# Optimization experiments

Hardware: AMD Instinct MI355X
Metric: run time of the kernel (lower is better)

Reference implementation:

```python
import jax, jax.numpy as jnp
import numpy as np

N_NODES = 10000
N_EDGES = 320000


def gcn_conv(x, edge_index, edge_weight, W, b):
    """PyG GCNConv (add_self_loops=True, normalize=True) with edge weights.
    x: [N, Fin], edge_index: [2, E] (row=source, col=target), W: [Fin, Fout].
    """
    n = x.shape[0]
    row, col = edge_index[0], edge_index[1]
    # add self-loops with weight 1
    loop = jnp.arange(n, dtype=edge_index.dtype)
    row = jnp.concatenate([row, loop])
    col = jnp.concatenate([col, loop])
    ew = jnp.concatenate([edge_weight, jnp.ones((n,), dtype=edge_weight.dtype)])
    # symmetric normalization: D^-1/2 A D^-1/2
    deg = jax.ops.segment_sum(ew, col, num_segments=n)
    dinv = jnp.where(deg > 0, jax.lax.rsqrt(deg), 0.0)
    norm = dinv[row] * ew * dinv[col]  # [E+N]
    # linear transform first (smaller of the two widths often), then aggregate
    xw = x @ W  # [N, Fout]
    msg = norm[:, None] * xw[row]  # [E+N, Fout] gather
    out = jax.ops.segment_sum(msg, col, num_segments=n)  # scatter-add
    return out + b


def setup_inputs() -> dict:
    key = jax.random.key(0)
    ks = jax.random.split(key, 8)
    F = 256
    x = jax.random.normal(ks[0], (N_NODES, F), dtype=jnp.float32)
    edge_index = jax.random.randint(ks[1], (2, N_EDGES), 0, N_NODES, dtype=jnp.int64)
    edge_weights = jax.random.uniform(ks[2], (N_EDGES,), dtype=jnp.float32)
    s1 = 1.0 / np.sqrt(F)
    s2 = 1.0 / np.sqrt(2 * F)
    s3 = 1.0 / np.sqrt(3 * F)
    W1 = jax.random.normal(ks[3], (F, 2 * F), dtype=jnp.float32) * s1
    b1 = jnp.zeros((2 * F,), dtype=jnp.float32)
    W2 = jax.random.normal(ks[4], (2 * F, 3 * F), dtype=jnp.float32) * s2
    b2 = jnp.zeros((3 * F,), dtype=jnp.float32)
    W3 = jax.random.normal(ks[5], (3 * F, 8), dtype=jnp.float32) * s3
    b3 = jnp.zeros((8,), dtype=jnp.float32)
    return {"x": x, "edge_index": edge_index, "edge_weights": edge_weights,
            "W1": W1, "b1": b1, "W2": W2, "b2": b2, "W3": W3, "b3": b3}


def reference(x, edge_index, edge_weights, W1, b1, W2, b2, W3, b3):
    h = jax.nn.relu(gcn_conv(x, edge_index, edge_weights, W1, b1))
    h = jax.nn.relu(gcn_conv(h, edge_index, edge_weights, W2, b2))
    return gcn_conv(h, edge_index, edge_weights, W3, b3)
```

## Files before the change

### kernel.cpp

```cpp
#include <hip/hip_runtime.h>

#define N_NODES 10000
#define N_EDGES 320000
#define ELL_CAP 88
#define ELL_TOT (N_NODES * ELL_CAP)
#define CDL 8

__device__ __forceinline__ unsigned short f2h_bits(float v) {
    _Float16 h = (_Float16)v;
    unsigned short u;
    __builtin_memcpy(&u, &h, 2);
    return u;
}
__device__ __forceinline__ float h2f_lo(unsigned int g) {
    unsigned short u = (unsigned short)(g & 0xFFFFu);
    _Float16 h; __builtin_memcpy(&h, &u, 2);
    return (float)h;
}
__device__ __forceinline__ float h2f_hi(unsigned int g) {
    unsigned short u = (unsigned short)(g >> 16);
    _Float16 h; __builtin_memcpy(&h, &u, 2);
    return (float)h;
}

__device__ __forceinline__ int cd_cnt(unsigned long long v) { return (int)(v >> 32); }
__device__ __forceinline__ float cd_deg(unsigned long long v) {
    return 1.0f + (float)(unsigned int)(v & 0xFFFFFFFFull) * 5.9604645e-8f;
}

__global__ __launch_bounds__(256) void setup_kernel(
        unsigned long long* __restrict__ cda,
        uint2* __restrict__ ell_e,
        const float* __restrict__ x, unsigned short* __restrict__ xh,
        const float* __restrict__ W1, unsigned short* __restrict__ w1t,
        const float* __restrict__ W2, unsigned short* __restrict__ w2t) {
    int i = blockIdx.x * 256 + threadIdx.x;
    const int S0 = N_NODES;
    const int S1 = S0 + ELL_TOT;
    const int S2 = S1 + N_NODES * 256;
    const int S3 = S2 + 256 * 512;
    const int S4 = S3 + 512 * 768;
    if (i < S0) {
        cda[i * CDL] = 0ULL;
    } else if (i < S1) {
        int j = i - S0;
        uint2 z; z.x = 0u; z.y = 0u;
        ell_e[j] = z;
    } else if (i < S2) {
        int j = i - S1;
        xh[j] = f2h_bits(x[j]);
    } else if (i < S3) {
        int j = i - S2;
        int k = j >> 9, n = j & 511;
        w1t[n * 256 + k] = f2h_bits(W1[j]);
    } else if (i < S4) {
        int j = i - S3;
        int k = j / 768, n = j - k * 768;
        w2t[n * 512 + k] = f2h_bits(W2[j]);
    }
}

__global__ __launch_bounds__(256) void ell_fill_kernel(const int* __restrict__ row,
                                                       const int* __restrict__ col,
                                                       const float* __restrict__ ew,
                                                       unsigned long long* __restrict__ cda,
                                                       uint2* __restrict__ ell_e, int e) {
    int i = blockIdx.x * 256 + threadIdx.x;
    if (i < e) {
        int c = col[i];
        float w = ew[i];
        unsigned long long inc =
            (1ULL << 32) | (unsigned long long)__float2uint_rn(w * 16777216.0f);
        unsigned long long old = atomicAdd(cda + c * CDL, inc);
        int slot = (int)(old >> 32);
        if (slot < ELL_CAP) {
            uint2 p;
            p.x = (unsigned int)row[i];
            p.y = __float_as_uint(w);
            ell_e[c * ELL_CAP + slot] = p;
        }
    }
}

template <int F, int SSHIFT, bool RAW>
__global__ __launch_bounds__(256) void agg_ell_kernel(const unsigned int* __restrict__ xpk,
                                                      const unsigned long long* __restrict__ cda,
                                                      const uint2* __restrict__ ell_e,
                                                      uint2* __restrict__ ell_n,
                                                      unsigned int* __restrict__ o) {
    constexpr int F2 = F / 2;
    const int b = (int)blockIdx.x;
    const int slice = b & ((1 << SSHIFT) - 1);
    const int node = __builtin_amdgcn_readfirstlane(
        (b >> SSHIFT) * 4 + ((int)threadIdx.x >> 6));
    const int lane = (int)threadIdx.x & 63;
    const int f2 = slice * 64 + lane;
    const unsigned long long cv = cda[node * CDL];
    const float srn = rsqrtf(cd_deg(cv));
    const float si = srn * srn;
    unsigned int gs = xpk[node * F2 + f2];
    float acc0 = si * h2f_lo(gs);
    float acc1 = si * h2f_hi(gs);
    const int base = node * ELL_CAP;
    int cnt8 = (cd_cnt(cv) + 7) & ~7;
    if (cnt8 > ELL_CAP) cnt8 = ELL_CAP;

    const int* meta = (const int*)(RAW ? ell_e : (const uint2*)ell_n);

    for (int j = 0; j < cnt8; j += 8) {
        const int* ep = meta + (size_t)(base + j) * 2;
        int4 a0 = *(const int4*)(ep + 0);
        int4 a1 = *(const int4*)(ep + 4);
        int4 a2 = *(const int4*)(ep + 8);
        int4 a3 = *(const int4*)(ep + 12);
        unsigned int g0 = xpk[a0.x * F2 + f2];
        unsigned int g1 = xpk[a0.z * F2 + f2];
        unsigned int g2 = xpk[a1.x * F2 + f2];
        unsigned int g3 = xpk[a1.z * F2 + f2];
        unsigned int g4 = xpk[a2.x * F2 + f2];
        unsigned int g5 = xpk[a2.z * F2 + f2];
        unsigned int g6 = xpk[a3.x * F2 + f2];
        unsigned int g7 = xpk[a3.z * F2 + f2];

        float w0, w1, w2, w3, w4, w5, w6, w7;
        if constexpr (RAW) {
            w0 = rsqrtf(cd_deg(cda[a0.x * CDL])) * __int_as_float(a0.y) * srn;
            w1 = rsqrtf(cd_deg(cda[a0.z * CDL])) * __int_as_float(a0.w) * srn;
            w2 = rsqrtf(cd_deg(cda[a1.x * CDL])) * __int_as_float(a1.y) * srn;
            w3 = rsqrtf(cd_deg(cda[a1.z * CDL])) * __int_as_float(a1.w) * srn;
            w4 = rsqrtf(cd_deg(cda[a2.x * CDL])) * __int_as_float(a2.y) * srn;
            w5 = rsqrtf(cd_deg(cda[a2.z * CDL])) * __int_as_float(a2.w) * srn;
            w6 = rsqrtf(cd_deg(cda[a3.x * CDL])) * __int_as_float(a3.y) * srn;
            w7 = rsqrtf(cd_deg(cda[a3.z * CDL])) * __int_as_float(a3.w) * srn;
            if (slice == 0 && lane == 0) {
                uint2* wp = ell_n + base + j;
                uint2 p;
                p.x = (unsigned int)a0.x; p.y = __float_as_uint(w0); wp[0] = p;
                p.x = (unsigned int)a0.z; p.y = __float_as_uint(w1); wp[1] = p;
                p.x = (unsigned int)a1.x; p.y = __float_as_uint(w2); wp[2] = p;
                p.x = (unsigned int)a1.z; p.y = __float_as_uint(w3); wp[3] = p;
                p.x = (unsigned int)a2.x; p.y = __float_as_uint(w4); wp[4] = p;
                p.x = (unsigned int)a2.z; p.y = __float_as_uint(w5); wp[5] = p;
                p.x = (unsigned int)a3.x; p.y = __float_as_uint(w6); wp[6] = p;
                p.x = (unsigned int)a3.z; p.y = __float_as_uint(w7); wp[7] = p;
            }
        } else {
            w0 = __int_as_float(a0.y); w1 = __int_as_float(a0.w);
            w2 = __int_as_float(a1.y); w3 = __int_as_float(a1.w);
            w4 = __int_as_float(a2.y); w5 = __int_as_float(a2.w);
            w6 = __int_as_float(a3.y); w7 = __int_as_float(a3.w);
        }

        acc0 += w0 * h2f_lo(g0) + w1 * h2f_lo(g1) + w2 * h2f_lo(g2) + w3 * h2f_lo(g3);
        acc1 += w0 * h2f_hi(g0) + w1 * h2f_hi(g1) + w2 * h2f_hi(g2) + w3 * h2f_hi(g3);
        acc0 += w4 * h2f_lo(g4) + w5 * h2f_lo(g5) + w6 * h2f_lo(g6) + w7 * h2f_lo(g7);
        acc1 += w4 * h2f_hi(g4) + w5 * h2f_hi(g5) + w6 * h2f_hi(g6) + w7 * h2f_hi(g7);
    }

    unsigned short h0 = f2h_bits(acc0);
    unsigned short h1 = f2h_bits(acc1);
    o[node * F2 + f2] = ((unsigned int)h1 << 16) | h0;
}

typedef _Float16 half8 __attribute__((ext_vector_type(8)));
typedef float f32x4 __attribute__((ext_vector_type(4)));

#define TM 128
#define TN 128
#define BK 32
#define LDS_A 0
#define LDS_B 8192
#define LDS_BUF 16384

__device__ __forceinline__ void async16(const unsigned short* g, unsigned char* l) {
    __builtin_amdgcn_global_load_lds(
        (const __attribute__((address_space(1))) unsigned int*)g,
        (__attribute__((address_space(3))) unsigned int*)l, 16, 0, 0);
}

__global__ __launch_bounds__(256, 3) void gemm_mfma_kernel(
        const unsigned short* __restrict__ A,
        const unsigned short* __restrict__ Bt,
        const float* __restrict__ bias,
        unsigned short* __restrict__ Cb,
        int M, int K, int N) {
    __shared__ unsigned char lds[2 * LDS_BUF];
    const int t = (int)threadIdx.x;

    const int gx = (int)gridDim.x;
    const int nwg = gx * (int)gridDim.y;
    const int lin = (int)blockIdx.y * gx + (int)blockIdx.x;
    const int xcd = lin & 7, idx = lin >> 3;
    const int q = nwg >> 3, r = nwg & 7;
    const int logi = (xcd < r ? xcd * (q + 1) : r * (q + 1) + (xcd - r) * q) + idx;
    const int bm = (logi / gx) * TM;
    const int bn = (logi % gx) * TN;

    const int lane = t & 63;
    const int wave = t >> 6;
    const int wm = (wave & 1) * 64;
    const int wn = (wave >> 1) * 64;

    const int slr = lane >> 2;
    const int scc = (lane & 3) ^ ((slr >> 1) & 3);
    const int bi0 = wave * 2, bi1 = wave * 2 + 1;
    const unsigned short* gA0 = A + (size_t)(bm + bi0 * 16 + slr) * K + scc * 8;
    const unsigned short* gA1 = A + (size_t)(bm + bi1 * 16 + slr) * K + scc * 8;
    const unsigned short* gB0 = Bt + (size_t)(bn + bi0 * 16 + slr) * K + scc * 8;
    const unsigned short* gB1 = Bt + (size_t)(bn + bi1 * 16 + slr) * K + scc * 8;

    const int quad = lane >> 4;
    const int lr16 = lane & 15;
    const int fs = (quad ^ ((lr16 >> 1) & 3)) * 16;

    f32x4 acc[4][4];
    const f32x4 zero4 = {0.f, 0.f, 0.f, 0.f};
#pragma unroll
    for (int i = 0; i < 4; ++i)
#pragma unroll
        for (int j = 0; j < 4; ++j) acc[i][j] = zero4;

    const int KT = K / BK;

    auto stage = [&](int kt, int buf) {
        const int k0 = kt * BK;
        unsigned char* b = &lds[buf * LDS_BUF];
        async16(gA0 + k0, b + LDS_A + bi0 * 1024);
        async16(gA1 + k0, b + LDS_A + bi1 * 1024);
        async16(gB0 + k0, b + LDS_B + bi0 * 1024);
        async16(gB1 + k0, b + LDS_B + bi1 * 1024);
    };

    stage(0, 0);
    __syncthreads();

    for (int kt = 0; kt < KT; ++kt) {
        const int buf = kt & 1;
        if (kt + 1 < KT) stage(kt + 1, buf ^ 1);

        unsigned char* b = &lds[buf * LDS_BUF];
        half8 av[4], bv[4];
#pragma unroll
        for (int i = 0; i < 4; ++i) {
            int ro = (wm + i * 16 + lr16) * 64 + fs;
            av[i] = *(const half8*)(b + LDS_A + ro);
        }
#pragma unroll
        for (int j = 0; j < 4; ++j) {
            int ro = (wn + j * 16 + lr16) * 64 + fs;
            bv[j] = *(const half8*)(b + LDS_B + ro);
        }
#pragma unroll
        for (int i = 0; i < 4; ++i)
#pragma unroll
            for (int j = 0; j < 4; ++j)
                acc[i][j] = __builtin_amdgcn_mfma_f32_16x16x32_f16(av[i], bv[j], acc[i][j], 0, 0, 0);
        __syncthreads();
    }

    float bcol[4];
#pragma unroll
    for (int j = 0; j < 4; ++j) bcol[j] = bias[bn + wn + j * 16 + lr16];
#pragma unroll
    for (int i = 0; i < 4; ++i) {
#pragma unroll
        for (int r2 = 0; r2 < 4; ++r2) {
            int m = bm + wm + i * 16 + quad * 4 + r2;
            if (m < M) {
#pragma unroll
                for (int j = 0; j < 4; ++j) {
                    float vv = fmaxf(acc[i][j][r2] + bcol[j], 0.f);
                    Cb[(size_t)m * N + bn + wn + j * 16 + lr16] = f2h_bits(vv);
                }
            }
        }
    }
}

__global__ __launch_bounds__(64) void gemm_n8_kernel(const unsigned int* __restrict__ Apk,
                                                     const float* __restrict__ B,
                                                     float* __restrict__ C) {
    const int m = blockIdx.x;
    const int lane = (int)threadIdx.x;
    const unsigned int* a = Apk + m * 384;
    float acc[8] = {};
#pragma unroll
    for (int it = 0; it < 6; ++it) {
        int j2 = lane + it * 64;
        unsigned int av = a[j2];
        float a0 = h2f_lo(av), a1 = h2f_hi(av);
        const float* B0 = B + (size_t)(2 * j2) * 8;
        float4 p0 = *(const float4*)(B0);
        float4 p1 = *(const float4*)(B0 + 4);
        float4 q0 = *(const float4*)(B0 + 8);
        float4 q1 = *(const float4*)(B0 + 12);
        acc[0] += a0 * p0.x + a1 * q0.x; acc[1] += a0 * p0.y + a1 * q0.y;
        acc[2] += a0 * p0.z + a1 * q0.z; acc[3] += a0 * p0.w + a1 * q0.w;
        acc[4] += a0 * p1.x + a1 * q1.x; acc[5] += a0 * p1.y + a1 * q1.y;
        acc[6] += a0 * p1.z + a1 * q1.z; acc[7] += a0 * p1.w + a1 * q1.w;
    }
#pragma unroll
    for (int off = 32; off > 0; off >>= 1) {
#pragma unroll
        for (int i = 0; i < 8; ++i) acc[i] += __shfl_down(acc[i], off);
    }
    if (lane == 0) {
#pragma unroll
        for (int i = 0; i < 8; ++i) C[(size_t)m * 8 + i] = acc[i];
    }
}

__global__ __launch_bounds__(64) void agg8_kernel(const float* __restrict__ xw,
                                                  const unsigned long long* __restrict__ cda,
                                                  const uint2* __restrict__ ell_n,
                                                  const float* __restrict__ bias,
                                                  float* __restrict__ out) {
    int node = blockIdx.x;
    int lane = threadIdx.x;
    float acc[8] = {};
    const int base = node * ELL_CAP;
    const unsigned long long cv = cda[node * CDL];
    int cnt = cd_cnt(cv);
    if (cnt > ELL_CAP) cnt = ELL_CAP;
    for (int j = lane; j < cnt; j += 64) {
        uint2 p = ell_n[base + j];
        int src = (int)p.x;
        float w = __uint_as_float(p.y);
        float4 g0 = *(const float4*)(xw + (size_t)src * 8);
        float4 g1 = *(const float4*)(xw + (size_t)src * 8 + 4);
        acc[0] += w * g0.x; acc[1] += w * g0.y; acc[2] += w * g0.z; acc[3] += w * g0.w;
        acc[4] += w * g1.x; acc[5] += w * g1.y; acc[6] += w * g1.z; acc[7] += w * g1.w;
    }
#pragma unroll
    for (int off = 32; off > 0; off >>= 1) {
#pragma unroll
        for (int i = 0; i < 8; ++i) acc[i] += __shfl_down(acc[i], off);
    }
    if (lane == 0) {
        float si = 1.0f / cd_deg(cv);
#pragma unroll
        for (int i = 0; i < 8; ++i)
            out[(size_t)node * 8 + i] = acc[i] + si * xw[(size_t)node * 8 + i] + bias[i];
    }
}


extern "C" void kernel_launch(void* const* d_in, const int* in_sizes, int n_in,
                              void* d_out, int out_size, void* d_ws, size_t ws_size,
                              hipStream_t stream) {
    const int N = N_NODES, E = N_EDGES;
    const int N_PAD = ((N + TM - 1) / TM) * TM;
    const float* x   = (const float*)d_in[0];
    const int*   ei  = (const int*)d_in[1];
    const float* ew  = (const float*)d_in[2];
    const float* W1  = (const float*)d_in[3];
    const float* b1  = (const float*)d_in[4];
    const float* W2  = (const float*)d_in[5];
    const float* b2  = (const float*)d_in[6];
    const float* W3  = (const float*)d_in[7];
    const float* b3  = (const float*)d_in[8];
    float* out = (float*)d_out;

    const int* row = ei;
    const int* col = ei + E;

    char* ws = (char*)d_ws;
    size_t off = 0;
    auto alloc = [&](size_t bytes) {
        void* p = ws + off;
        off += (bytes + 255) & ~(size_t)255;
        return p;
    };
    unsigned long long* cda = (unsigned long long*)alloc((size_t)N * CDL * 8);
    uint2*          ell_e   = (uint2*)alloc((size_t)ELL_TOT * 8);
    uint2*          ell_n   = (uint2*)alloc((size_t)ELL_TOT * 8);
    unsigned short* xh      = (unsigned short*)alloc((size_t)N * 256 * 2);
    unsigned short* h1h     = (unsigned short*)alloc((size_t)N * 512 * 2);
    unsigned short* h2h     = (unsigned short*)alloc((size_t)N * 768 * 2);
    unsigned short* Aagg    = (unsigned short*)alloc((size_t)N_PAD * 512 * 2);
    unsigned short* W1t     = (unsigned short*)alloc((size_t)512 * 256 * 2);
    unsigned short* W2t     = (unsigned short*)alloc((size_t)768 * 512 * 2);
    float*          xw8     = (float*)alloc((size_t)N * 8 * 4);
    (void)ws_size;

    {
        int tot = N + ELL_TOT + N * 256 + 256 * 512 + 512 * 768;
        setup_kernel<<<(tot + 255) / 256, 256, 0, stream>>>(
            cda, ell_e, x, xh, W1, W1t, W2, W2t);
    }
    ell_fill_kernel<<<(E + 255) / 256, 256, 0, stream>>>(row, col, ew, cda, ell_e, E);

    agg_ell_kernel<256, 1, true><<<N * 2 / 4, 256, 0, stream>>>(
        (const unsigned int*)xh, cda, ell_e, ell_n, (unsigned int*)Aagg);
    {
        dim3 grid(512 / TN, N_PAD / TM);
        gemm_mfma_kernel<<<grid, 256, 0, stream>>>(Aagg, W1t, b1, h1h, N, 256, 512);
    }
    agg_ell_kernel<512, 2, false><<<N * 4 / 4, 256, 0, stream>>>(
        (const unsigned int*)h1h, cda, ell_n, ell_n, (unsigned int*)Aagg);
    {
        dim3 grid(768 / TN, N_PAD / TM);
        gemm_mfma_kernel<<<grid, 256, 0, stream>>>(Aagg, W2t, b2, h2h, N, 512, 768);
    }
    gemm_n8_kernel<<<N, 64, 0, stream>>>((const unsigned int*)h2h, W3, xw8);
    agg8_kernel<<<N, 64, 0, stream>>>(xw8, cda, ell_n, b3, out);

    (void)out_size; (void)n_in; (void)in_sizes;
}
```

Before: 202.2 us.

## Fuse layer-3 W3 projection into layer-2 GEMM epilogue with partial sums

The layer-2 MFMA GEMM epilogue now multiplies its ReLU output tile by the matching rows of W3. It reduces across lanes and waves through shuffles and LDS, and writes per-column-tile partial 8-wide projections. This removes the fp16 h2 intermediate write/read and the separate gemm_n8 launch. The final aggregation kernel now sums six partial buffers per gathered source, which multiplies its gather traffic. The epilogue also contains some dead statements.

Measured after the change: 203.1 us. No clear change (+0.4%).

```diff
diff --git a/kernel.cpp b/kernel.cpp
--- a/kernel.cpp
+++ b/kernel.cpp
@@ -171,6 +171,7 @@
 #define LDS_A 0
 #define LDS_B 8192
 #define LDS_BUF 16384
+#define NP 10112
 
 __device__ __forceinline__ void async16(const unsigned short* g, unsigned char* l) {
     __builtin_amdgcn_global_load_lds(
@@ -178,11 +179,14 @@
         (__attribute__((address_space(3))) unsigned int*)l, 16, 0, 0);
 }
 
+template <bool FUSE_W3>
 __global__ __launch_bounds__(256, 3) void gemm_mfma_kernel(
         const unsigned short* __restrict__ A,
         const unsigned short* __restrict__ Bt,
         const float* __restrict__ bias,
         unsigned short* __restrict__ Cb,
+        const float* __restrict__ W3,
+        float* __restrict__ xw8p,
         int M, int K, int N) {
     __shared__ unsigned char lds[2 * LDS_BUF];
     const int t = (int)threadIdx.x;
@@ -261,56 +265,99 @@
     float bcol[4];
 #pragma unroll
     for (int j = 0; j < 4; ++j) bcol[j] = bias[bn + wn + j * 16 + lr16];
-#pragma unroll
-    for (int i = 0; i < 4; ++i) {
-#pragma unroll
-        for (int r2 = 0; r2 < 4; ++r2) {
-            int m = bm + wm + i * 16 + quad * 4 + r2;
-            if (m < M) {
+
+    if constexpr (!FUSE_W3) {
+#pragma unroll
+        for (int i = 0; i < 4; ++i) {
+#pragma unroll
+            for (int r2 = 0; r2 < 4; ++r2) {
+                int m = bm + wm + i * 16 + quad * 4 + r2;
+                if (m < M) {
+#pragma unroll
+                    for (int j = 0; j < 4; ++j) {
+                        float vv = fmaxf(acc[i][j][r2] + bcol[j], 0.f);
+                        Cb[(size_t)m * N + bn + wn + j * 16 + lr16] = f2h_bits(vv);
+                    }
+                }
+            }
+        }
+    } else {
+        const int ct = bn / TN;
+        float* red = (float*)lds;
+        float4 w3a[4], w3b[4];
+#pragma unroll
+        for (int j = 0; j < 4; ++j) {
+            const float* wr = W3 + (size_t)(bn + wn + j * 16 + lr16) * 8;
+            w3a[j] = *(const float4*)wr;
+            w3b[j] = *(const float4*)(wr + 4);
+        }
+#pragma unroll
+        for (int i = 0; i < 4; ++i) {
+#pragma unroll
+            for (int r2 = 0; r2 < 4; ++r2) {
+                float s0 = 0.f, s1 = 0.f, s2 = 0.f, s3 = 0.f;
+                float s4 = 0.f, s5 = 0.f, s6 = 0.f, s7 = 0.f;
 #pragma unroll
                 for (int j = 0; j < 4; ++j) {
                     float vv = fmaxf(acc[i][j][r2] + bcol[j], 0.f);
-                    Cb[(size_t)m * N + bn + wn + j * 16 + lr16] = f2h_bits(vv);
+                    s0 += vv * w3a[j].x; s1 += vv * w3a[j].y;
+                    s2 += vv * w3a[j].z; s3 += vv * w3a[j].w;
+                    s4 += vv * w3b[j].x; s5 += vv * w3b[j].y;
+                    s6 += vv * w3b[j].z; s7 += vv * w3b[j].w;
+                }
+#pragma unroll
+                for (int mk = 1; mk < 16; mk <<= 1) {
+                    s0 += __shfl_xor(s0, mk); s1 += __shfl_xor(s1, mk);
+                    s2 += __shfl_xor(s2, mk); s3 += __shfl_xor(s3, mk);
+                    s4 += __shfl_xor(s4, mk); s5 += __shfl_xor(s5, mk);
+                    s6 += __shfl_xor(s6, mk); s7 += __shfl_xor(s7, mk);
+                }
+                if (wn == 64 && lr16 == 0) {
+                    int rl = wm + i * 16 + quad * 4 + r2;
+                    float* rp = red + rl * 8;
+                    rp[0] = s0; rp[1] = s1; rp[2] = s2; rp[3] = s3;
+                    rp[4] = s4; rp[5] = s5; rp[6] = s6; rp[7] = s7;
+                }
+                acc[i][0][r2] = s0; acc[i][1][r2] = s1;
+                acc[i][2][r2] = s2; acc[i][3][r2] = s3;
+                bcol[0] = bcol[0];
+                if (wn == 0) {
+                }
+                if (wn == 0 && lr16 == 0) {
+                    int rl = wm + i * 16 + quad * 4 + r2;
+                    float* rp = red + 1024 + rl * 8;
+                    rp[0] = s4; rp[1] = s5; rp[2] = s6; rp[3] = s7;
                 }
             }
         }
-    }
-}
-
-__global__ __launch_bounds__(64) void gemm_n8_kernel(const unsigned int* __restrict__ Apk,
-                                                     const float* __restrict__ B,
-                                                     float* __restrict__ C) {
-    const int m = blockIdx.x;
-    const int lane = (int)threadIdx.x;
-    const unsigned int* a = Apk + m * 384;
-    float acc[8] = {};
-#pragma unroll
-    for (int it = 0; it < 6; ++it) {
-        int j2 = lane + it * 64;
-        unsigned int av = a[j2];
-        float a0 = h2f_lo(av), a1 = h2f_hi(av);
-        const float* B0 = B + (size_t)(2 * j2) * 8;
-        float4 p0 = *(const float4*)(B0);
-        float4 p1 = *(const float4*)(B0 + 4);
-        float4 q0 = *(const float4*)(B0 + 8);
-        float4 q1 = *(const float4*)(B0 + 12);
-        acc[0] += a0 * p0.x + a1 * q0.x; acc[1] += a0 * p0.y + a1 * q0.y;
-        acc[2] += a0 * p0.z + a1 * q0.z; acc[3] += a0 * p0.w + a1 * q0.w;
-        acc[4] += a0 * p1.x + a1 * q1.x; acc[5] += a0 * p1.y + a1 * q1.y;
-        acc[6] += a0 * p1.z + a1 * q1.z; acc[7] += a0 * p1.w + a1 * q1.w;
-    }
-#pragma unroll
-    for (int off = 32; off > 0; off >>= 1) {
-#pragma unroll
-        for (int i = 0; i < 8; ++i) acc[i] += __shfl_down(acc[i], off);
-    }
-    if (lane == 0) {
-#pragma unroll
-        for (int i = 0; i < 8; ++i) C[(size_t)m * 8 + i] = acc[i];
-    }
-}
-
-__global__ __launch_bounds__(64) void agg8_kernel(const float* __restrict__ xw,
+        __syncthreads();
+        if (wn == 0 && lr16 == 0) {
+#pragma unroll
+            for (int i = 0; i < 4; ++i) {
+#pragma unroll
+                for (int r2 = 0; r2 < 4; ++r2) {
+                    int rl = wm + i * 16 + quad * 4 + r2;
+                    int m = bm + rl;
+                    if (m < M) {
+                        const float* pp = red + rl * 8;
+                        const float* sp = red + 1024 + rl * 8;
+                        float* xp = xw8p + ((size_t)ct * NP + m) * 8;
+                        xp[0] = acc[i][0][r2] + pp[0];
+                        xp[1] = acc[i][1][r2] + pp[1];
+                        xp[2] = acc[i][2][r2] + pp[2];
+                        xp[3] = acc[i][3][r2] + pp[3];
+                        xp[4] = sp[0] + pp[4];
+                        xp[5] = sp[1] + pp[5];
+                        xp[6] = sp[2] + pp[6];
+                        xp[7] = sp[3] + pp[7];
+                    }
+                }
+            }
+        }
+    }
+}
+
+__global__ __launch_bounds__(64) void agg8_kernel(const float* __restrict__ xw8p,
                                                   const unsigned long long* __restrict__ cda,
                                                   const uint2* __restrict__ ell_n,
                                                   const float* __restrict__ bias,
@@ -326,10 +373,18 @@
         uint2 p = ell_n[base + j];
         int src = (int)p.x;
         float w = __uint_as_float(p.y);
-        float4 g0 = *(const float4*)(xw + (size_t)src * 8);
-        float4 g1 = *(const float4*)(xw + (size_t)src * 8 + 4);
-        acc[0] += w * g0.x; acc[1] += w * g0.y; acc[2] += w * g0.z; acc[3] += w * g0.w;
-        acc[4] += w * g1.x; acc[5] += w * g1.y; acc[6] += w * g1.z; acc[7] += w * g1.w;
+        float s0 = 0.f, s1 = 0.f, s2 = 0.f, s3 = 0.f;
+        float s4 = 0.f, s5 = 0.f, s6 = 0.f, s7 = 0.f;
+#pragma unroll
+        for (int ct = 0; ct < 6; ++ct) {
+            const float* xp = xw8p + ((size_t)ct * NP + src) * 8;
+            float4 g0 = *(const float4*)xp;
+            float4 g1 = *(const float4*)(xp + 4);
+            s0 += g0.x; s1 += g0.y; s2 += g0.z; s3 += g0.w;
+            s4 += g1.x; s5 += g1.y; s6 += g1.z; s7 += g1.w;
+        }
+        acc[0] += w * s0; acc[1] += w * s1; acc[2] += w * s2; acc[3] += w * s3;
+        acc[4] += w * s4; acc[5] += w * s5; acc[6] += w * s6; acc[7] += w * s7;
     }
 #pragma unroll
     for (int off = 32; off > 0; off >>= 1) {
@@ -338,9 +393,18 @@
     }
     if (lane == 0) {
         float si = 1.0f / cd_deg(cv);
+        float self[8];
+#pragma unroll
+        for (int i = 0; i < 8; ++i) self[i] = 0.f;
+#pragma unroll
+        for (int ct = 0; ct < 6; ++ct) {
+            const float* xp = xw8p + ((size_t)ct * NP + node) * 8;
+#pragma unroll
+            for (int i = 0; i < 8; ++i) self[i] += xp[i];
+        }
 #pragma unroll
         for (int i = 0; i < 8; ++i)
-            out[(size_t)node * 8 + i] = acc[i] + si * xw[(size_t)node * 8 + i] + bias[i];
+            out[(size_t)node * 8 + i] = acc[i] + si * self[i] + bias[i];
     }
 }
 
@@ -349,7 +413,6 @@
                               void* d_out, int out_size, void* d_ws, size_t ws_size,
                               hipStream_t stream) {
     const int N = N_NODES, E = N_EDGES;
-    const int N_PAD = ((N + TM - 1) / TM) * TM;
     const float* x   = (const float*)d_in[0];
     const int*   ei  = (const int*)d_in[1];
     const float* ew  = (const float*)d_in[2];
@@ -376,11 +439,10 @@
     uint2*          ell_n   = (uint2*)alloc((size_t)ELL_TOT * 8);
     unsigned short* xh      = (unsigned short*)alloc((size_t)N * 256 * 2);
     unsigned short* h1h     = (unsigned short*)alloc((size_t)N * 512 * 2);
-    unsigned short* h2h     = (unsigned short*)alloc((size_t)N * 768 * 2);
-    unsigned short* Aagg    = (unsigned short*)alloc((size_t)N_PAD * 512 * 2);
+    unsigned short* Aagg    = (unsigned short*)alloc((size_t)NP * 512 * 2);
     unsigned short* W1t     = (unsigned short*)alloc((size_t)512 * 256 * 2);
     unsigned short* W2t     = (unsigned short*)alloc((size_t)768 * 512 * 2);
-    float*          xw8     = (float*)alloc((size_t)N * 8 * 4);
+    float*          xw8p    = (float*)alloc((size_t)6 * NP * 8 * 4);
     (void)ws_size;
 
     {
@@ -393,17 +455,18 @@
     agg_ell_kernel<256, 1, true><<<N * 2 / 4, 256, 0, stream>>>(
         (const unsigned int*)xh, cda, ell_e, ell_n, (unsigned int*)Aagg);
     {
-        dim3 grid(512 / TN, N_PAD / TM);
-        gemm_mfma_kernel<<<grid, 256, 0, stream>>>(Aagg, W1t, b1, h1h, N, 256, 512);
+        dim3 grid(512 / TN, NP / TM);
+        gemm_mfma_kernel<false><<<grid, 256, 0, stream>>>(
+            Aagg, W1t, b1, h1h, nullptr, nullptr, N, 256, 512);
     }
     agg_ell_kernel<512, 2, false><<<N * 4 / 4, 256, 0, stream>>>(
         (const unsigned int*)h1h, cda, ell_n, ell_n, (unsigned int*)Aagg);
     {
-        dim3 grid(768 / TN, N_PAD / TM);
-        gemm_mfma_kernel<<<grid, 256, 0, stream>>>(Aagg, W2t, b2, h2h, N, 512, 768);
-    }
-    gemm_n8_kernel<<<N, 64, 0, stream>>>((const unsigned int*)h2h, W3, xw8);
-    agg8_kernel<<<N, 64, 0, stream>>>(xw8, cda, ell_n, b3, out);
+        dim3 grid(768 / TN, NP / TM);
+        gemm_mfma_kernel<true><<<grid, 256, 0, stream>>>(
+            Aagg, W2t, b2, nullptr, W3, xw8p, N, 512, 768);
+    }
+    agg8_kernel<<<N, 64, 0, stream>>>(xw8p, cda, ell_n, b3, out);
 
     (void)out_size; (void)n_in; (void)in_sizes;
 }
```

## Skip ELL zero-fill and unroll aggregation by 16 with masked tail

Applied to the files above, without the earlier changes.

Drops the setup pass that zeroed the whole ELL edge buffer. The first aggregation now masks padding slots in its tail iteration and writes zeros into the normalized ELL copy itself. The main gather loop is unrolled to 16 neighbors per iteration to put more independent loads in flight, with an 8-wide masked tail. This removes roughly 7 MB of memory writes from setup, at the cost of more registers and extra tail logic. Later layers depend on ell_n padding being written as zeros.

After: 202.0 us. Within noise of the previous version (-0.1%).

```diff
diff --git a/kernel.cpp b/kernel.cpp
--- a/kernel.cpp
+++ b/kernel.cpp
@@ -30,31 +30,25 @@
 
 __global__ __launch_bounds__(256) void setup_kernel(
         unsigned long long* __restrict__ cda,
-        uint2* __restrict__ ell_e,
         const float* __restrict__ x, unsigned short* __restrict__ xh,
         const float* __restrict__ W1, unsigned short* __restrict__ w1t,
         const float* __restrict__ W2, unsigned short* __restrict__ w2t) {
     int i = blockIdx.x * 256 + threadIdx.x;
     const int S0 = N_NODES;
-    const int S1 = S0 + ELL_TOT;
-    const int S2 = S1 + N_NODES * 256;
-    const int S3 = S2 + 256 * 512;
-    const int S4 = S3 + 512 * 768;
+    const int S1 = S0 + N_NODES * 256;
+    const int S2 = S1 + 256 * 512;
+    const int S3 = S2 + 512 * 768;
     if (i < S0) {
         cda[i * CDL] = 0ULL;
     } else if (i < S1) {
         int j = i - S0;
-        uint2 z; z.x = 0u; z.y = 0u;
-        ell_e[j] = z;
+        xh[j] = f2h_bits(x[j]);
     } else if (i < S2) {
         int j = i - S1;
-        xh[j] = f2h_bits(x[j]);
+        int k = j >> 9, n = j & 511;
+        w1t[n * 256 + k] = f2h_bits(W1[j]);
     } else if (i < S3) {
         int j = i - S2;
-        int k = j >> 9, n = j & 511;
-        w1t[n * 256 + k] = f2h_bits(W1[j]);
-    } else if (i < S4) {
-        int j = i - S3;
         int k = j / 768, n = j - k * 768;
         w2t[n * 512 + k] = f2h_bits(W2[j]);
     }
@@ -102,17 +96,22 @@
     float acc0 = si * h2f_lo(gs);
     float acc1 = si * h2f_hi(gs);
     const int base = node * ELL_CAP;
-    int cnt8 = (cd_cnt(cv) + 7) & ~7;
-    if (cnt8 > ELL_CAP) cnt8 = ELL_CAP;
+    int cnt = cd_cnt(cv);
+    if (cnt > ELL_CAP) cnt = ELL_CAP;
 
     const int* meta = (const int*)(RAW ? ell_e : (const uint2*)ell_n);
 
-    for (int j = 0; j < cnt8; j += 8) {
+    int j = 0;
+    for (; j + 16 <= cnt; j += 16) {
         const int* ep = meta + (size_t)(base + j) * 2;
         int4 a0 = *(const int4*)(ep + 0);
         int4 a1 = *(const int4*)(ep + 4);
         int4 a2 = *(const int4*)(ep + 8);
         int4 a3 = *(const int4*)(ep + 12);
+        int4 a4 = *(const int4*)(ep + 16);
+        int4 a5 = *(const int4*)(ep + 20);
+        int4 a6 = *(const int4*)(ep + 24);
+        int4 a7 = *(const int4*)(ep + 28);
         unsigned int g0 = xpk[a0.x * F2 + f2];
         unsigned int g1 = xpk[a0.z * F2 + f2];
         unsigned int g2 = xpk[a1.x * F2 + f2];
@@ -121,8 +120,16 @@
         unsigned int g5 = xpk[a2.z * F2 + f2];
         unsigned int g6 = xpk[a3.x * F2 + f2];
         unsigned int g7 = xpk[a3.z * F2 + f2];
-
-        float w0, w1, w2, w3, w4, w5, w6, w7;
+        unsigned int g8 = xpk[a4.x * F2 + f2];
+        unsigned int g9 = xpk[a4.z * F2 + f2];
+        unsigned int gA = xpk[a5.x * F2 + f2];
+        unsigned int gB = xpk[a5.z * F2 + f2];
+        unsigned int gC = xpk[a6.x * F2 + f2];
+        unsigned int gD = xpk[a6.z * F2 + f2];
+        unsigned int gE = xpk[a7.x * F2 + f2];
+        unsigned int gF = xpk[a7.z * F2 + f2];
+
+        float w0, w1, w2, w3, w4, w5, w6, w7, w8, w9, wA, wB, wC, wD, wE, wF;
         if constexpr (RAW) {
             w0 = rsqrtf(cd_deg(cda[a0.x * CDL])) * __int_as_float(a0.y) * srn;
             w1 = rsqrtf(cd_deg(cda[a0.z * CDL])) * __int_as_float(a0.w) * srn;
@@ -132,25 +139,111 @@
             w5 = rsqrtf(cd_deg(cda[a2.z * CDL])) * __int_as_float(a2.w) * srn;
             w6 = rsqrtf(cd_deg(cda[a3.x * CDL])) * __int_as_float(a3.y) * srn;
             w7 = rsqrtf(cd_deg(cda[a3.z * CDL])) * __int_as_float(a3.w) * srn;
+            w8 = rsqrtf(cd_deg(cda[a4.x * CDL])) * __int_as_float(a4.y) * srn;
+            w9 = rsqrtf(cd_deg(cda[a4.z * CDL])) * __int_as_float(a4.w) * srn;
+            wA = rsqrtf(cd_deg(cda[a5.x * CDL])) * __int_as_float(a5.y) * srn;
+            wB = rsqrtf(cd_deg(cda[a5.z * CDL])) * __int_as_float(a5.w) * srn;
+            wC = rsqrtf(cd_deg(cda[a6.x * CDL])) * __int_as_float(a6.y) * srn;
+            wD = rsqrtf(cd_deg(cda[a6.z * CDL])) * __int_as_float(a6.w) * srn;
+            wE = rsqrtf(cd_deg(cda[a7.x * CDL])) * __int_as_float(a7.y) * srn;
+            wF = rsqrtf(cd_deg(cda[a7.z * CDL])) * __int_as_float(a7.w) * srn;
             if (slice == 0 && lane == 0) {
                 uint2* wp = ell_n + base + j;
                 uint2 p;
-                p.x = (unsigned int)a0.x; p.y = __float_as_uint(w0); wp[0] = p;
-                p.x = (unsigned int)a0.z; p.y = __float_as_uint(w1); wp[1] = p;
-                p.x = (unsigned int)a1.x; p.y = __float_as_uint(w2); wp[2] = p;
-                p.x = (unsigned int)a1.z; p.y = __float_as_uint(w3); wp[3] = p;
-                p.x = (unsigned int)a2.x; p.y = __float_as_uint(w4); wp[4] = p;
-                p.x = (unsigned int)a2.z; p.y = __float_as_uint(w5); wp[5] = p;
-                p.x = (unsigned int)a3.x; p.y = __float_as_uint(w6); wp[6] = p;
-                p.x = (unsigned int)a3.z; p.y = __float_as_uint(w7); wp[7] = p;
+                p.x = (unsigned int)a0.x; p.y = __float_as_uint(w0); wp[0]  = p;
+                p.x = (unsigned int)a0.z; p.y = __float_as_uint(w1); wp[1]  = p;
+                p.x = (unsigned int)a1.x; p.y = __float_as_uint(w2); wp[2]  = p;
+                p.x = (unsigned int)a1.z; p.y = __float_as_uint(w3); wp[3]  = p;
+                p.x = (unsigned int)a2.x; p.y = __float_as_uint(w4); wp[4]  = p;
+                p.x = (unsigned int)a2.z; p.y = __float_as_uint(w5); wp[5]  = p;
+                p.x = (unsigned int)a3.x; p.y = __float_as_uint(w6); wp[6]  = p;
+                p.x = (unsigned int)a3.z; p.y = __float_as_uint(w7); wp[7]  = p;
+                p.x = (unsigned int)a4.x; p.y = __float_as_uint(w8); wp[8]  = p;
+                p.x = (unsigned int)a4.z; p.y = __float_as_uint(w9); wp[9]  = p;
+                p.x = (unsigned int)a5.x; p.y = __float_as_uint(wA); wp[10] = p;
+                p.x = (unsigned int)a5.z; p.y = __float_as_uint(wB); wp[11] = p;
+                p.x = (unsigned int)a6.x; p.y = __float_as_uint(wC); wp[12] = p;
+                p.x = (unsigned int)a6.z; p.y = __float_as_uint(wD); wp[13] = p;
+                p.x = (unsigned int)a7.x; p.y = __float_as_uint(wE); wp[14] = p;
+                p.x = (unsigned int)a7.z; p.y = __float_as_uint(wF); wp[15] = p;
             }
         } else {
             w0 = __int_as_float(a0.y); w1 = __int_as_float(a0.w);
             w2 = __int_as_float(a1.y); w3 = __int_as_float(a1.w);
             w4 = __int_as_float(a2.y); w5 = __int_as_float(a2.w);
             w6 = __int_as_float(a3.y); w7 = __int_as_float(a3.w);
+            w8 = __int_as_float(a4.y); w9 = __int_as_float(a4.w);
+            wA = __int_as_float(a5.y); wB = __int_as_float(a5.w);
+            wC = __int_as_float(a6.y); wD = __int_as_float(a6.w);
+            wE = __int_as_float(a7.y); wF = __int_as_float(a7.w);
         }
 
+        acc0 += w0 * h2f_lo(g0) + w1 * h2f_lo(g1) + w2 * h2f_lo(g2) + w3 * h2f_lo(g3);
+        acc1 += w0 * h2f_hi(g0) + w1 * h2f_hi(g1) + w2 * h2f_hi(g2) + w3 * h2f_hi(g3);
+        acc0 += w4 * h2f_lo(g4) + w5 * h2f_lo(g5) + w6 * h2f_lo(g6) + w7 * h2f_lo(g7);
+        acc1 += w4 * h2f_hi(g4) + w5 * h2f_hi(g5) + w6 * h2f_hi(g6) + w7 * h2f_hi(g7);
+        acc0 += w8 * h2f_lo(g8) + w9 * h2f_lo(g9) + wA * h2f_lo(gA) + wB * h2f_lo(gB);
+        acc1 += w8 * h2f_hi(g8) + w9 * h2f_hi(g9) + wA * h2f_hi(gA) + wB * h2f_hi(gB);
+        acc0 += wC * h2f_lo(gC) + wD * h2f_lo(gD) + wE * h2f_lo(gE) + wF * h2f_lo(gF);
+        acc1 += wC * h2f_hi(gC) + wD * h2f_hi(gD) + wE * h2f_hi(gE) + wF * h2f_hi(gF);
+    }
+
+    for (; j < cnt; j += 8) {
+        const int* ep = meta + (size_t)(base + j) * 2;
+        int4 a0 = *(const int4*)(ep + 0);
+        int4 a1 = *(const int4*)(ep + 4);
+        int4 a2 = *(const int4*)(ep + 8);
+        int4 a3 = *(const int4*)(ep + 12);
+
+        int s0, s1, s2, s3, s4, s5, s6, s7;
+        float w0, w1, w2, w3, w4, w5, w6, w7;
+        if constexpr (RAW) {
+            s0 = (j + 0 < cnt) ? a0.x : 0;  float r0 = (j + 0 < cnt) ? __int_as_float(a0.y) : 0.f;
+            s1 = (j + 1 < cnt) ? a0.z : 0;  float r1 = (j + 1 < cnt) ? __int_as_float(a0.w) : 0.f;
+            s2 = (j + 2 < cnt) ? a1.x : 0;  float r2 = (j + 2 < cnt) ? __int_as_float(a1.y) : 0.f;
+            s3 = (j + 3 < cnt) ? a1.z : 0;  float r3 = (j + 3 < cnt) ? __int_as_float(a1.w) : 0.f;
+            s4 = (j + 4 < cnt) ? a2.x : 0;  float r4 = (j + 4 < cnt) ? __int_as_float(a2.y) : 0.f;
+            s5 = (j + 5 < cnt) ? a2.z : 0;  float r5 = (j + 5 < cnt) ? __int_as_float(a2.w) : 0.f;
+            s6 = (j + 6 < cnt) ? a3.x : 0;  float r6 = (j + 6 < cnt) ? __int_as_float(a3.y) : 0.f;
+            s7 = (j + 7 < cnt) ? a3.z : 0;  float r7 = (j + 7 < cnt) ? __int_as_float(a3.w) : 0.f;
+            w0 = rsqrtf(cd_deg(cda[s0 * CDL])) * r0 * srn;
+            w1 = rsqrtf(cd_deg(cda[s1 * CDL])) * r1 * srn;
+            w2 = rsqrtf(cd_deg(cda[s2 * CDL])) * r2 * srn;
+            w3 = rsqrtf(cd_deg(cda[s3 * CDL])) * r3 * srn;
+            w4 = rsqrtf(cd_deg(cda[s4 * CDL])) * r4 * srn;
+            w5 = rsqrtf(cd_deg(cda[s5 * CDL])) * r5 * srn;
+            w6 = rsqrtf(cd_deg(cda[s6 * CDL])) * r6 * srn;
+            w7 = rsqrtf(cd_deg(cda[s7 * CDL])) * r7 * srn;
+            if (slice == 0 && lane == 0) {
+                uint2* wp = ell_n + base + j;
+                uint2 p;
+                p.x = (unsigned int)s0; p.y = __float_as_uint(w0); wp[0] = p;
+                p.x = (unsigned int)s1; p.y = __float_as_uint(w1); wp[1] = p;
+                p.x = (unsigned int)s2; p.y = __float_as_uint(w2); wp[2] = p;
+                p.x = (unsigned int)s3; p.y = __float_as_uint(w3); wp[3] = p;
+                p.x = (unsigned int)s4; p.y = __float_as_uint(w4); wp[4] = p;
+                p.x = (unsigned int)s5; p.y = __float_as_uint(w5); wp[5] = p;
+                p.x = (unsigned int)s6; p.y = __float_as_uint(w6); wp[6] = p;
+                p.x = (unsigned int)s7; p.y = __float_as_uint(w7); wp[7] = p;
+            }
+        } else {
+            s0 = a0.x; w0 = __int_as_float(a0.y);
+            s1 = a0.z; w1 = __int_as_float(a0.w);
+            s2 = a1.x; w2 = __int_as_float(a1.y);
+            s3 = a1.z; w3 = __int_as_float(a1.w);
+            s4 = a2.x; w4 = __int_as_float(a2.y);
+            s5 = a2.z; w5 = __int_as_float(a2.w);
+            s6 = a3.x; w6 = __int_as_float(a3.y);
+            s7 = a3.z; w7 = __int_as_float(a3.w);
+        }
+        unsigned int g0 = xpk[s0 * F2 + f2];
+        unsigned int g1 = xpk[s1 * F2 + f2];
+        unsigned int g2 = xpk[s2 * F2 + f2];
+        unsigned int g3 = xpk[s3 * F2 + f2];
+        unsigned int g4 = xpk[s4 * F2 + f2];
+        unsigned int g5 = xpk[s5 * F2 + f2];
+        unsigned int g6 = xpk[s6 * F2 + f2];
+        unsigned int g7 = xpk[s7 * F2 + f2];
         acc0 += w0 * h2f_lo(g0) + w1 * h2f_lo(g1) + w2 * h2f_lo(g2) + w3 * h2f_lo(g3);
         acc1 += w0 * h2f_hi(g0) + w1 * h2f_hi(g1) + w2 * h2f_hi(g2) + w3 * h2f_hi(g3);
         acc0 += w4 * h2f_lo(g4) + w5 * h2f_lo(g5) + w6 * h2f_lo(g6) + w7 * h2f_lo(g7);
@@ -384,9 +477,9 @@
     (void)ws_size;
 
     {
-        int tot = N + ELL_TOT + N * 256 + 256 * 512 + 512 * 768;
+        int tot = N + N * 256 + 256 * 512 + 512 * 768;
         setup_kernel<<<(tot + 255) / 256, 256, 0, stream>>>(
-            cda, ell_e, x, xh, W1, W1t, W2, W2t);
+            cda, x, xh, W1, W1t, W2, W2t);
     }
     ell_fill_kernel<<<(E + 255) / 256, 256, 0, stream>>>(row, col, ew, cda, ell_e, E);
 
```
